# Kernel optimization log

Measured on AMD Instinct MI355X. Metric: run time of the kernel, lower is better.

The kernel has to match this reference:

```python
import jax, jax.numpy as jnp
import numpy as np

D_MODEL = 1024
N_HEADS = 16
D_K = D_MODEL // N_HEADS
B, S = 8, 1024
EPS = 1e-8


def setup_inputs() -> dict:
    key = jax.random.key(0)
    ks = jax.random.split(key, 6)
    scale = 1.0 / np.sqrt(D_MODEL)
    return {
        "Q_in": jax.random.normal(ks[0], (B, S, D_MODEL), jnp.float32),
        "mask": jax.random.randint(ks[1], (B, 1, S, S), 0, 2, jnp.int32),
        "Wq": jax.random.normal(ks[2], (D_MODEL, D_MODEL), jnp.float32) * scale,
        "bq": jnp.zeros((D_MODEL,), jnp.float32),
        "Wk": jax.random.normal(ks[3], (D_MODEL, D_MODEL), jnp.float32) * scale,
        "bk": jnp.zeros((D_MODEL,), jnp.float32),
        "Wv": jax.random.normal(ks[4], (D_MODEL, D_MODEL), jnp.float32) * scale,
        "bv": jnp.zeros((D_MODEL,), jnp.float32),
        "Wo": jax.random.normal(ks[5], (D_MODEL, D_MODEL), jnp.float32) * scale,
        "bo": jnp.zeros((D_MODEL,), jnp.float32),
    }


def reference(Q_in, mask, Wq, bq, Wk, bk, Wv, bv, Wo, bo):
    # QKV projections: [B,S,D] -> [B,H,S,d_k]
    def split_heads(x):
        return x.reshape(B, S, N_HEADS, D_K).transpose(0, 2, 1, 3)

    Q = split_heads(Q_in @ Wq + bq)
    K = split_heads(Q_in @ Wk + bk)
    V = split_heads(Q_in @ Wv + bv)

    # scaled scores [B,H,S,S], standard softmax
    scores = jnp.einsum("bhqd,bhkd->bhqk", Q, K) / jnp.sqrt(
        jnp.asarray(D_K, jnp.float32))
    scores = jax.nn.softmax(scores, axis=-1)
    # non-standard: multiplicative mask AFTER softmax, then row renorm
    scores = scores * mask.astype(scores.dtype)
    attn = scores / (jnp.sum(scores, axis=-1, keepdims=True) + EPS)

    context = jnp.einsum("bhqk,bhkd->bhqd", attn, V)
    context = context.transpose(0, 2, 1, 3).reshape(B, S, D_MODEL)
    return context @ Wo + bo
```

## Files before the change

kernel.cpp:

```cpp
#include <hip/hip_runtime.h>
#include <hip/hip_bf16.h>
#include <stdint.h>

typedef __attribute__((ext_vector_type(4))) float f32x4;
typedef __attribute__((ext_vector_type(8))) __bf16 bf16x8;
typedef unsigned short u16;
typedef unsigned int u32;
typedef unsigned long long u64;

#define NH 16
#define DKK 64

__device__ __forceinline__ u16 f2bf(float f) {
    u32 u = __builtin_bit_cast(u32, f);
    u32 r = (u + 0x7fffu + ((u >> 16) & 1u)) >> 16;
    return (u16)r;
}

__device__ __forceinline__ u16 cvt_bf(float f) {
    __hip_bfloat16 h = __float2bfloat16(f);
    return *reinterpret_cast<u16*>(&h);
}

__device__ __forceinline__ void gload16(const void* g, void* l) {
    __builtin_amdgcn_global_load_lds((const __attribute__((address_space(1))) void*)g,
                                     (__attribute__((address_space(3))) void*)l, 16, 0, 0);
}

__global__ __launch_bounds__(256) void k_convert_x(const float* __restrict__ x,
                                                   u16* __restrict__ xb) {
    int i = blockIdx.x * 256 + threadIdx.x;
    const float4* p = (const float4*)x + (size_t)i * 2;
    float4 a = p[0], b = p[1];
    union { u16 h[8]; uint4 q; } o;
    o.h[0] = f2bf(a.x); o.h[1] = f2bf(a.y); o.h[2] = f2bf(a.z); o.h[3] = f2bf(a.w);
    o.h[4] = f2bf(b.x); o.h[5] = f2bf(b.y); o.h[6] = f2bf(b.z); o.h[7] = f2bf(b.w);
    ((uint4*)xb)[i] = o.q;
}

__global__ __launch_bounds__(256) void k_convert_w(const float* __restrict__ wq,
                                                   const float* __restrict__ wk,
                                                   const float* __restrict__ wv,
                                                   const float* __restrict__ wo,
                                                   u16* __restrict__ wt) {
    int z = blockIdx.z;
    const float* w = (z == 0) ? wq : (z == 1) ? wk : (z == 2) ? wv : wo;
    __shared__ float t[32][33];
    int tx = threadIdx.x & 31, ty = threadIdx.x >> 5;
    int n0 = blockIdx.x * 32, k0 = blockIdx.y * 32;
    for (int rr = 0; rr < 4; ++rr)
        t[ty + rr * 8][tx] = w[(size_t)(k0 + ty + rr * 8) * 1024 + n0 + tx];
    __syncthreads();
    for (int rr = 0; rr < 4; ++rr) {
        int n = n0 + ty + rr * 8;
        wt[((size_t)z * 1024 + n) * 1024 + k0 + tx] = f2bf(t[tx][ty + rr * 8]);
    }
}

__global__ __launch_bounds__(256) void k_maskpack(const int* __restrict__ mask,
                                                  u64* __restrict__ mb) {
    int wid = (blockIdx.x * 256 + threadIdx.x) >> 6;
    int lane = threadIdx.x & 63;
    for (int c = wid; c < 8 * 1024 * 16; c += 8192) {
        int m = mask[(size_t)c * 64 + lane];
        u64 bits = __ballot(m != 0);
        if (lane == 0)
            mb[(c & 0xFFFFC000u) | ((c & 15) << 10) | ((c >> 4) & 1023)] = bits;
    }
}

template <int MODE>
__global__ __launch_bounds__(256) void k_gemm(const u16* __restrict__ A,
                                              const u16* __restrict__ Bt,
                                              const float* __restrict__ b0,
                                              const float* __restrict__ b1,
                                              const float* __restrict__ b2,
                                              u16* __restrict__ q_out,
                                              u16* __restrict__ k_out,
                                              u16* __restrict__ v_out,
                                              float* __restrict__ out) {
    __shared__ u16 As[128 * 32];
    __shared__ u16 Bs[128 * 32];
    int tid = threadIdx.x;
    int wv = tid >> 6, lane = tid & 63;
    int r = lane & 15, g = lane >> 4;
    int wr = wv >> 1, wc = wv & 1;
    int m0 = blockIdx.x * 128, n0 = blockIdx.y * 128;
    f32x4 acc[4][4] = {};
    for (int kt = 0; kt < 1024; kt += 32) {
        __syncthreads();
        for (int i = 0; i < 2; ++i) {
            int e = i * 256 + tid;
            int row = e >> 2;
            int cs = ((e & 3) ^ ((row >> 1) & 3)) * 8;
            const u16* ga = A + (size_t)(m0 + row) * 1024 + kt + cs;
            const u16* gb = Bt + (size_t)(n0 + row) * 1024 + kt + cs;
            gload16(ga, As + (size_t)(i * 256 + wv * 64) * 8);
            gload16(gb, Bs + (size_t)(i * 256 + wv * 64) * 8);
        }
        __syncthreads();
        bf16x8 aF[4], bF[4];
#pragma unroll
        for (int m = 0; m < 4; ++m) {
            int ro = wr * 64 + m * 16 + r;
            aF[m] = *(const bf16x8*)&As[ro * 32 + ((g ^ ((ro >> 1) & 3)) << 3)];
        }
#pragma unroll
        for (int n = 0; n < 4; ++n) {
            int ro = wc * 64 + n * 16 + r;
            bF[n] = *(const bf16x8*)&Bs[ro * 32 + ((g ^ ((ro >> 1) & 3)) << 3)];
        }
#pragma unroll
        for (int m = 0; m < 4; ++m)
#pragma unroll
            for (int n = 0; n < 4; ++n)
                acc[m][n] = __builtin_amdgcn_mfma_f32_16x16x32_bf16(aF[m], bF[n], acc[m][n], 0, 0, 0);
    }
    for (int m = 0; m < 4; ++m) {
        int rowb = m0 + wr * 64 + m * 16 + 4 * g;
        for (int n = 0; n < 4; ++n) {
            int col = n0 + wc * 64 + n * 16 + r;
            if (MODE == 0) {
                int w = col >> 10, cn = col & 1023;
                const float* bp = (w == 0) ? b0 : (w == 1) ? b1 : b2;
                u16* dst = (w == 0) ? q_out : (w == 1) ? k_out : v_out;
                float sc = (w == 0) ? 0.125f : 1.0f;
                int h = cn >> 6, d = cn & 63;
                float bias = bp[cn];
                for (int i = 0; i < 4; ++i) {
                    int row = rowb + i;
                    int b = row >> 10, s = row & 1023;
                    float v = (acc[m][n][i] + bias) * sc;
                    dst[((size_t)(b * NH + h) * 1024 + s) * 64 + d] = f2bf(v);
                }
            } else {
                float bias = b0[col];
                for (int i = 0; i < 4; ++i) {
                    int row = rowb + i;
                    out[(size_t)row * 1024 + col] = acc[m][n][i] + bias;
                }
            }
        }
    }
}

__global__ __launch_bounds__(256) void k_transpose_v(const u16* __restrict__ vb,
                                                     u16* __restrict__ vt) {
    __shared__ u16 t[64][72];
    int bh = blockIdx.y, s0 = blockIdx.x * 64;
    int tid = threadIdx.x;
    for (int i = 0; i < 2; ++i) {
        int e = i * 256 + tid;
        int row = e >> 3, ch = (e & 7) * 8;
        uint4 v = *(const uint4*)(vb + ((size_t)bh * 1024 + s0 + row) * 64 + ch);
        *(uint4*)&t[row][ch] = v;
    }
    __syncthreads();
    for (int i = 0; i < 2; ++i) {
        int e = i * 256 + tid;
        int d = e >> 3, ch = (e & 7) * 8;
        union { u16 h[8]; uint4 q; } o;
        for (int j = 0; j < 8; ++j) o.h[j] = t[ch + j][d];
        *(uint4*)(vt + ((size_t)bh * 64 + d) * 1024 + s0 + ch) = o.q;
    }
}

__global__ __launch_bounds__(256, 3) void k_attn(const u16* __restrict__ qb,
                                                 const u16* __restrict__ kb,
                                                 const u16* __restrict__ vt,
                                                 const u64* __restrict__ mbits,
                                                 u16* __restrict__ ctx) {
    __shared__ u16 Kd[2][64 * 64];
    __shared__ u16 Vd[2][64 * 64];
    int tid = threadIdx.x, wv = tid >> 6, lane = tid & 63;
    int r = lane & 15, g = lane >> 4;
    int q0 = blockIdx.x * 128, bh = blockIdx.y;
    int b = bh >> 4, h = bh & 15;

    bf16x8 aq[2][2];
    for (int qg = 0; qg < 2; ++qg) {
        const u16* qp = qb + ((size_t)bh * 1024 + q0 + wv * 32 + qg * 16 + r) * 64 + g * 8;
        aq[qg][0] = *(const bf16x8*)qp;
        aq[qg][1] = *(const bf16x8*)(qp + 32);
    }

    f32x4 of[2][4] = {};
    f32x4 zacc[2] = {};
    const bf16x8 vone = {(__bf16)1.f, (__bf16)1.f, (__bf16)1.f, (__bf16)1.f,
                         (__bf16)1.f, (__bf16)1.f, (__bf16)1.f, (__bf16)1.f};

    const u64* mrow = mbits + ((size_t)b * 16) * 1024 + q0 + wv * 32 + r;
    u64 mbc[2] = {mrow[0], mrow[16]};

    for (int i2 = 0; i2 < 2; ++i2) {
        int e = i2 * 256 + tid;
        int s = e >> 3, c = e & 7;
        int cs = (c ^ (s & 7)) * 8;
        int kr = (s & 0x20) | ((s & 0x0C) << 1) | ((s & 0x10) >> 2) | (s & 3);
        gload16(kb + ((size_t)bh * 1024 + kr) * 64 + cs, Kd[0] + (size_t)e * 8);
        gload16(vt + ((size_t)bh * 64 + s) * 1024 + cs, Vd[0] + (size_t)e * 8);
    }
    __syncthreads();

    for (int t = 0; t < 16; ++t) {
        int cur = t & 1;
        u64 mbn0 = 0, mbn1 = 0;
        if (t < 15) {
            int ktn = (t + 1) * 64;
            for (int i2 = 0; i2 < 2; ++i2) {
                int e = i2 * 256 + tid;
                int s = e >> 3, c = e & 7;
                int cs = (c ^ (s & 7)) * 8;
                int kr = (s & 0x20) | ((s & 0x0C) << 1) | ((s & 0x10) >> 2) | (s & 3);
                gload16(kb + ((size_t)bh * 1024 + ktn + kr) * 64 + cs, Kd[cur ^ 1] + (size_t)e * 8);
                gload16(vt + ((size_t)bh * 64 + s) * 1024 + ktn + cs, Vd[cur ^ 1] + (size_t)e * 8);
            }
            mbn0 = mrow[(size_t)(t + 1) * 1024];
            mbn1 = mrow[(size_t)(t + 1) * 1024 + 16];
        }
        const u16* K = Kd[cur];
        const u16* V = Vd[cur];

        bf16x8 bk0[4], bk1[4];
#pragma unroll
        for (int nf = 0; nf < 4; ++nf) {
            int rowk = (nf * 16 + r) * 64;
            bk0[nf] = *(const bf16x8*)&K[rowk + ((g ^ (r & 7)) << 3)];
            bk1[nf] = *(const bf16x8*)&K[rowk + (((g + 4) ^ (r & 7)) << 3)];
        }

        bf16x8 pfr[2][2];
#pragma unroll
        for (int qg = 0; qg < 2; ++qg) {
            f32x4 sf[4];
#pragma unroll
            for (int nf = 0; nf < 4; ++nf) {
                f32x4 z = {0.f, 0.f, 0.f, 0.f};
                z = __builtin_amdgcn_mfma_f32_16x16x32_bf16(bk0[nf], aq[qg][0], z, 0, 0, 0);
                sf[nf] = __builtin_amdgcn_mfma_f32_16x16x32_bf16(bk1[nf], aq[qg][1], z, 0, 0, 0);
            }
            u64 m64 = mbc[qg] >> (g * 8);
            u32 mlo = (u32)m64, mhi = (u32)(m64 >> 32);
            u32 pw[8];
#pragma unroll
            for (int nf = 0; nf < 4; ++nf) {
                u32 nib = ((nf & 2) ? mhi : mlo) >> ((nf & 1) * 4);
                u32 pm0 = ((nib & 1) ? 0xFFFFu : 0u) | ((nib & 2) ? 0xFFFF0000u : 0u);
                u32 pm1 = ((nib & 4) ? 0xFFFFu : 0u) | ((nib & 8) ? 0xFFFF0000u : 0u);
                float e0 = __expf(sf[nf][0]), e1 = __expf(sf[nf][1]);
                float e2 = __expf(sf[nf][2]), e3 = __expf(sf[nf][3]);
                pw[2 * nf]     = (((u32)cvt_bf(e0)) | ((u32)cvt_bf(e1) << 16)) & pm0;
                pw[2 * nf + 1] = (((u32)cvt_bf(e2)) | ((u32)cvt_bf(e3) << 16)) & pm1;
            }
            union { u32 w[4]; bf16x8 v; } f0, f1;
            f0.w[0] = pw[0]; f0.w[1] = pw[1]; f0.w[2] = pw[2]; f0.w[3] = pw[3];
            f1.w[0] = pw[4]; f1.w[1] = pw[5]; f1.w[2] = pw[6]; f1.w[3] = pw[7];
            pfr[qg][0] = f0.v;
            pfr[qg][1] = f1.v;
            zacc[qg] = __builtin_amdgcn_mfma_f32_16x16x32_bf16(vone, pfr[qg][0], zacc[qg], 0, 0, 0);
            zacc[qg] = __builtin_amdgcn_mfma_f32_16x16x32_bf16(vone, pfr[qg][1], zacc[qg], 0, 0, 0);
        }
#pragma unroll
        for (int ks = 0; ks < 2; ++ks) {
#pragma unroll
            for (int nf = 0; nf < 4; ++nf) {
                bf16x8 av = *(const bf16x8*)&V[(nf * 16 + r) * 64 + (((ks * 4 + g) ^ (r & 7)) << 3)];
                of[0][nf] = __builtin_amdgcn_mfma_f32_16x16x32_bf16(av, pfr[0][ks], of[0][nf], 0, 0, 0);
                of[1][nf] = __builtin_amdgcn_mfma_f32_16x16x32_bf16(av, pfr[1][ks], of[1][nf], 0, 0, 0);
            }
        }
        mbc[0] = mbn0;
        mbc[1] = mbn1;
        __syncthreads();
    }

    for (int qg = 0; qg < 2; ++qg) {
        float inv = 1.0f / zacc[qg][0];
        int qrow = q0 + wv * 32 + qg * 16 + r;
        u16* crow = ctx + ((size_t)(b * 1024 + qrow)) * 1024 + h * 64;
#pragma unroll
        for (int nf = 0; nf < 4; ++nf) {
            u32 w0 = ((u32)cvt_bf(of[qg][nf][0] * inv)) | ((u32)cvt_bf(of[qg][nf][1] * inv) << 16);
            u32 w1 = ((u32)cvt_bf(of[qg][nf][2] * inv)) | ((u32)cvt_bf(of[qg][nf][3] * inv) << 16);
            *(u32*)(crow + nf * 16 + g * 4) = w0;
            *(u32*)(crow + nf * 16 + g * 4 + 2) = w1;
        }
    }
}

extern "C" void kernel_launch(void* const* d_in, const int* in_sizes, int n_in,
                              void* d_out, int out_size, void* d_ws, size_t ws_size,
                              hipStream_t stream) {
    const float* Q_in = (const float*)d_in[0];
    const int*   mask = (const int*)d_in[1];
    const float* Wq = (const float*)d_in[2];
    const float* bq = (const float*)d_in[3];
    const float* Wk = (const float*)d_in[4];
    const float* bk = (const float*)d_in[5];
    const float* Wv = (const float*)d_in[6];
    const float* bv = (const float*)d_in[7];
    const float* Wo = (const float*)d_in[8];
    const float* bo = (const float*)d_in[9];

    char* ws = (char*)d_ws;
    u16* Xb = (u16*)(ws);
    u16* Wt = (u16*)(ws + 16777216);
    u16* Qb = (u16*)(ws + 25165824);
    u16* Kb = (u16*)(ws + 41943040);
    u16* Vb = (u16*)(ws + 58720256);
    u16* Vt = (u16*)(ws + 75497472);
    u64* Mb = (u64*)(ws + 92274688);
    u16* Ctx = Vb;

    k_convert_x<<<4096, 256, 0, stream>>>(Q_in, Xb);
    k_convert_w<<<dim3(32, 32, 4), 256, 0, stream>>>(Wq, Wk, Wv, Wo, Wt);
    k_maskpack<<<2048, 256, 0, stream>>>(mask, Mb);
    k_gemm<0><<<dim3(64, 24), 256, 0, stream>>>(Xb, Wt, bq, bk, bv, Qb, Kb, Vb, nullptr);
    k_transpose_v<<<dim3(16, 128), 256, 0, stream>>>(Vb, Vt);
    k_attn<<<dim3(8, 128), 256, 0, stream>>>(Qb, Kb, Vt, Mb, Ctx);
    k_gemm<1><<<dim3(64, 8), 256, 0, stream>>>(Ctx, Wt + (size_t)3 * 1024 * 1024,
                                               bo, nullptr, nullptr,
                                               nullptr, nullptr, nullptr, (float*)d_out);
}
```

Measured before the change: 176.7 us.

## Triple-buffer K/V tiles in attention with partial vmcnt waits and MFMA priority

Extends the attention kernel's K/V shared-memory staging from double to triple buffering, so each tile is prefetched two iterations ahead. Full __syncthreads is replaced with explicit s_waitcnt vmcnt(4) plus s_barrier, which keeps later loads in flight. Mask bits are preloaded once into registers and distributed with lane shuffles instead of a global load per iteration. s_setprio raises wave priority around MFMA sections. LDS use grows by half, which may reduce occupancy at the launch bound of 3 blocks.

```diff
diff --git a/kernel.cpp b/kernel.cpp
--- a/kernel.cpp
+++ b/kernel.cpp
@@ -170,110 +170,135 @@
                                                  const u16* __restrict__ vt,
                                                  const u64* __restrict__ mbits,
                                                  u16* __restrict__ ctx) {
-    __shared__ u16 Kd[2][64 * 64];
-    __shared__ u16 Vd[2][64 * 64];
+    __shared__ u16 Kd[3][64 * 64];
+    __shared__ u16 Vd[3][64 * 64];
     int tid = threadIdx.x, wv = tid >> 6, lane = tid & 63;
     int r = lane & 15, g = lane >> 4;
     int q0 = blockIdx.x * 128, bh = blockIdx.y;
     int b = bh >> 4, h = bh & 15;
 
     bf16x8 aq[2][2];
+#pragma unroll
     for (int qg = 0; qg < 2; ++qg) {
         const u16* qp = qb + ((size_t)bh * 1024 + q0 + wv * 32 + qg * 16 + r) * 64 + g * 8;
         aq[qg][0] = *(const bf16x8*)qp;
         aq[qg][1] = *(const bf16x8*)(qp + 32);
     }
 
+    const u64* mbase = mbits + (size_t)b * 16384 + q0 + wv * 32;
+    u64 mbq0[4], mbq1[4];
+#pragma unroll
+    for (int j = 0; j < 4; ++j) {
+        mbq0[j] = mbase[(size_t)(g * 4 + j) * 1024 + r];
+        mbq1[j] = mbase[(size_t)(g * 4 + j) * 1024 + 16 + r];
+    }
+
     f32x4 of[2][4] = {};
     f32x4 zacc[2] = {};
     const bf16x8 vone = {(__bf16)1.f, (__bf16)1.f, (__bf16)1.f, (__bf16)1.f,
                          (__bf16)1.f, (__bf16)1.f, (__bf16)1.f, (__bf16)1.f};
 
-    const u64* mrow = mbits + ((size_t)b * 16) * 1024 + q0 + wv * 32 + r;
-    u64 mbc[2] = {mrow[0], mrow[16]};
-
-    for (int i2 = 0; i2 < 2; ++i2) {
-        int e = i2 * 256 + tid;
-        int s = e >> 3, c = e & 7;
-        int cs = (c ^ (s & 7)) * 8;
-        int kr = (s & 0x20) | ((s & 0x0C) << 1) | ((s & 0x10) >> 2) | (s & 3);
-        gload16(kb + ((size_t)bh * 1024 + kr) * 64 + cs, Kd[0] + (size_t)e * 8);
-        gload16(vt + ((size_t)bh * 64 + s) * 1024 + cs, Vd[0] + (size_t)e * 8);
-    }
-    __syncthreads();
-
-    for (int t = 0; t < 16; ++t) {
-        int cur = t & 1;
-        u64 mbn0 = 0, mbn1 = 0;
-        if (t < 15) {
-            int ktn = (t + 1) * 64;
-            for (int i2 = 0; i2 < 2; ++i2) {
-                int e = i2 * 256 + tid;
-                int s = e >> 3, c = e & 7;
-                int cs = (c ^ (s & 7)) * 8;
-                int kr = (s & 0x20) | ((s & 0x0C) << 1) | ((s & 0x10) >> 2) | (s & 3);
-                gload16(kb + ((size_t)bh * 1024 + ktn + kr) * 64 + cs, Kd[cur ^ 1] + (size_t)e * 8);
-                gload16(vt + ((size_t)bh * 64 + s) * 1024 + ktn + cs, Vd[cur ^ 1] + (size_t)e * 8);
-            }
-            mbn0 = mrow[(size_t)(t + 1) * 1024];
-            mbn1 = mrow[(size_t)(t + 1) * 1024 + 16];
-        }
-        const u16* K = Kd[cur];
-        const u16* V = Vd[cur];
-
-        bf16x8 bk0[4], bk1[4];
-#pragma unroll
-        for (int nf = 0; nf < 4; ++nf) {
-            int rowk = (nf * 16 + r) * 64;
-            bk0[nf] = *(const bf16x8*)&K[rowk + ((g ^ (r & 7)) << 3)];
-            bk1[nf] = *(const bf16x8*)&K[rowk + (((g + 4) ^ (r & 7)) << 3)];
-        }
-
-        bf16x8 pfr[2][2];
-#pragma unroll
-        for (int qg = 0; qg < 2; ++qg) {
-            f32x4 sf[4];
+#define ATTN_STAGE(slot, ktn)                                                          \
+    {                                                                                  \
+        for (int i2 = 0; i2 < 2; ++i2) {                                               \
+            int e = i2 * 256 + tid;                                                    \
+            int s = e >> 3, c = e & 7;                                                 \
+            int cs = (c ^ (s & 7)) * 8;                                                \
+            int kr = (s & 0x20) | ((s & 0x0C) << 1) | ((s & 0x10) >> 2) | (s & 3);     \
+            gload16(kb + ((size_t)bh * 1024 + (ktn) + kr) * 64 + cs,                   \
+                    Kd[slot] + (size_t)e * 8);                                         \
+            gload16(vt + ((size_t)bh * 64 + s) * 1024 + (ktn) + cs,                    \
+                    Vd[slot] + (size_t)e * 8);                                         \
+        }                                                                              \
+    }
+
+    ATTN_STAGE(0, 0);
+    ATTN_STAGE(1, 64);
+    asm volatile("s_waitcnt vmcnt(4)" ::: "memory");
+    __builtin_amdgcn_s_barrier();
+
+    int cur = 0, s2 = 2;
+    for (int tt = 0; tt < 4; ++tt) {
+#pragma unroll
+        for (int j = 0; j < 4; ++j) {
+            int t = tt * 4 + j;
+            if (t < 14) ATTN_STAGE(s2, (t + 2) * 64);
+            const u16* K = Kd[cur];
+            const u16* V = Vd[cur];
+
+            int srcl = (tt << 4) + r;
+            u64 mb64[2];
+            mb64[0] = __shfl(mbq0[j], srcl, 64);
+            mb64[1] = __shfl(mbq1[j], srcl, 64);
+
+            bf16x8 bk0[4], bk1[4];
 #pragma unroll
             for (int nf = 0; nf < 4; ++nf) {
-                f32x4 z = {0.f, 0.f, 0.f, 0.f};
-                z = __builtin_amdgcn_mfma_f32_16x16x32_bf16(bk0[nf], aq[qg][0], z, 0, 0, 0);
-                sf[nf] = __builtin_amdgcn_mfma_f32_16x16x32_bf16(bk1[nf], aq[qg][1], z, 0, 0, 0);
-            }
-            u64 m64 = mbc[qg] >> (g * 8);
-            u32 mlo = (u32)m64, mhi = (u32)(m64 >> 32);
-            u32 pw[8];
-#pragma unroll
-            for (int nf = 0; nf < 4; ++nf) {
-                u32 nib = ((nf & 2) ? mhi : mlo) >> ((nf & 1) * 4);
-                u32 pm0 = ((nib & 1) ? 0xFFFFu : 0u) | ((nib & 2) ? 0xFFFF0000u : 0u);
-                u32 pm1 = ((nib & 4) ? 0xFFFFu : 0u) | ((nib & 8) ? 0xFFFF0000u : 0u);
-                float e0 = __expf(sf[nf][0]), e1 = __expf(sf[nf][1]);
-                float e2 = __expf(sf[nf][2]), e3 = __expf(sf[nf][3]);
-                pw[2 * nf]     = (((u32)cvt_bf(e0)) | ((u32)cvt_bf(e1) << 16)) & pm0;
-                pw[2 * nf + 1] = (((u32)cvt_bf(e2)) | ((u32)cvt_bf(e3) << 16)) & pm1;
-            }
-            union { u32 w[4]; bf16x8 v; } f0, f1;
-            f0.w[0] = pw[0]; f0.w[1] = pw[1]; f0.w[2] = pw[2]; f0.w[3] = pw[3];
-            f1.w[0] = pw[4]; f1.w[1] = pw[5]; f1.w[2] = pw[6]; f1.w[3] = pw[7];
-            pfr[qg][0] = f0.v;
-            pfr[qg][1] = f1.v;
-            zacc[qg] = __builtin_amdgcn_mfma_f32_16x16x32_bf16(vone, pfr[qg][0], zacc[qg], 0, 0, 0);
-            zacc[qg] = __builtin_amdgcn_mfma_f32_16x16x32_bf16(vone, pfr[qg][1], zacc[qg], 0, 0, 0);
-        }
-#pragma unroll
-        for (int ks = 0; ks < 2; ++ks) {
-#pragma unroll
-            for (int nf = 0; nf < 4; ++nf) {
-                bf16x8 av = *(const bf16x8*)&V[(nf * 16 + r) * 64 + (((ks * 4 + g) ^ (r & 7)) << 3)];
-                of[0][nf] = __builtin_amdgcn_mfma_f32_16x16x32_bf16(av, pfr[0][ks], of[0][nf], 0, 0, 0);
-                of[1][nf] = __builtin_amdgcn_mfma_f32_16x16x32_bf16(av, pfr[1][ks], of[1][nf], 0, 0, 0);
-            }
-        }
-        mbc[0] = mbn0;
-        mbc[1] = mbn1;
-        __syncthreads();
-    }
-
+                int rowk = (nf * 16 + r) * 64;
+                bk0[nf] = *(const bf16x8*)&K[rowk + ((g ^ (r & 7)) << 3)];
+                bk1[nf] = *(const bf16x8*)&K[rowk + (((g + 4) ^ (r & 7)) << 3)];
+            }
+
+            bf16x8 pfr[2][2];
+#pragma unroll
+            for (int qg = 0; qg < 2; ++qg) {
+                f32x4 sf[4];
+                __builtin_amdgcn_s_setprio(1);
+#pragma unroll
+                for (int nf = 0; nf < 4; ++nf) {
+                    f32x4 z = {0.f, 0.f, 0.f, 0.f};
+                    z = __builtin_amdgcn_mfma_f32_16x16x32_bf16(bk0[nf], aq[qg][0], z, 0, 0, 0);
+                    sf[nf] = __builtin_amdgcn_mfma_f32_16x16x32_bf16(bk1[nf], aq[qg][1], z, 0, 0, 0);
+                }
+                __builtin_amdgcn_s_setprio(0);
+                u64 m64 = mb64[qg] >> (g * 8);
+                u32 mlo = (u32)m64, mhi = (u32)(m64 >> 32);
+                u32 pw[8];
+#pragma unroll
+                for (int nf = 0; nf < 4; ++nf) {
+                    u32 nib = ((nf & 2) ? mhi : mlo) >> ((nf & 1) * 4);
+                    u32 pm0 = ((nib & 1) ? 0xFFFFu : 0u) | ((nib & 2) ? 0xFFFF0000u : 0u);
+                    u32 pm1 = ((nib & 4) ? 0xFFFFu : 0u) | ((nib & 8) ? 0xFFFF0000u : 0u);
+                    float e0 = __expf(sf[nf][0]), e1 = __expf(sf[nf][1]);
+                    float e2 = __expf(sf[nf][2]), e3 = __expf(sf[nf][3]);
+                    pw[2 * nf]     = (((u32)cvt_bf(e0)) | ((u32)cvt_bf(e1) << 16)) & pm0;
+                    pw[2 * nf + 1] = (((u32)cvt_bf(e2)) | ((u32)cvt_bf(e3) << 16)) & pm1;
+                }
+                union { u32 w[4]; bf16x8 v; } f0, f1;
+                f0.w[0] = pw[0]; f0.w[1] = pw[1]; f0.w[2] = pw[2]; f0.w[3] = pw[3];
+                f1.w[0] = pw[4]; f1.w[1] = pw[5]; f1.w[2] = pw[6]; f1.w[3] = pw[7];
+                pfr[qg][0] = f0.v;
+                pfr[qg][1] = f1.v;
+                __builtin_amdgcn_s_setprio(1);
+                zacc[qg] = __builtin_amdgcn_mfma_f32_16x16x32_bf16(vone, pfr[qg][0], zacc[qg], 0, 0, 0);
+                zacc[qg] = __builtin_amdgcn_mfma_f32_16x16x32_bf16(vone, pfr[qg][1], zacc[qg], 0, 0, 0);
+                __builtin_amdgcn_s_setprio(0);
+            }
+            __builtin_amdgcn_s_setprio(1);
+#pragma unroll
+            for (int ks = 0; ks < 2; ++ks) {
+#pragma unroll
+                for (int nf = 0; nf < 4; ++nf) {
+                    bf16x8 av = *(const bf16x8*)&V[(nf * 16 + r) * 64 + (((ks * 4 + g) ^ (r & 7)) << 3)];
+                    of[0][nf] = __builtin_amdgcn_mfma_f32_16x16x32_bf16(av, pfr[0][ks], of[0][nf], 0, 0, 0);
+                    of[1][nf] = __builtin_amdgcn_mfma_f32_16x16x32_bf16(av, pfr[1][ks], of[1][nf], 0, 0, 0);
+                }
+            }
+            __builtin_amdgcn_s_setprio(0);
+
+            if (t < 14) {
+                asm volatile("s_waitcnt vmcnt(4)" ::: "memory");
+                __builtin_amdgcn_s_barrier();
+            } else if (t == 14) {
+                asm volatile("s_waitcnt vmcnt(0)" ::: "memory");
+                __builtin_amdgcn_s_barrier();
+            }
+            cur = (cur == 2) ? 0 : cur + 1;
+            s2 = (s2 == 2) ? 0 : s2 + 1;
+        }
+    }
+
+#pragma unroll
     for (int qg = 0; qg < 2; ++qg) {
         float inv = 1.0f / zacc[qg][0];
         int qrow = q0 + wv * 32 + qg * 16 + r;
@@ -286,6 +311,7 @@
             *(u32*)(crow + nf * 16 + g * 4 + 2) = w1;
         }
     }
+#undef ATTN_STAGE
 }
 
 extern "C" void kernel_launch(void* const* d_in, const int* in_sizes, int n_in,
```

New measurement: 179.6 us. Within noise of the previous version (+1.7%).
